# Kernel tuning notes

Hardware: AMD Instinct MI355X
Metric: run time of the kernel (lower is better)

Reference implementation:

```python
import jax, jax.numpy as jnp
import numpy as np

B, T, C, H = 2, 2048, 2048, 16
HD = C // H  # head dim = 128


def setup_inputs() -> dict:
    key = jax.random.key(0)
    k1, k2, k3 = jax.random.split(key, 3)
    x = jax.random.normal(k1, (B, T, C), dtype=jnp.float32)
    # torch Linear stores weight as [out_features, in_features]; y = x @ W.T
    w_attn = jax.random.normal(k2, (3 * C, C), dtype=jnp.float32) * (C ** -0.5)
    w_proj = jax.random.normal(k3, (C, C), dtype=jnp.float32) * (C ** -0.5)
    b_proj = jnp.zeros((C,), dtype=jnp.float32)
    return {"x": x, "w_attn": w_attn, "w_proj": w_proj, "b_proj": b_proj}


def reference(x, w_attn, w_proj, b_proj):
    # c_attn: [B,T,C] -> [B,T,3C], then split into q,k,v
    qkv = jnp.einsum('btc,oc->bto', x, w_attn)
    q, k, v = jnp.split(qkv, 3, axis=-1)
    # [B,T,C] -> [B,H,T,HD]
    q = q.reshape(B, T, H, HD).transpose(0, 2, 1, 3)
    k = k.reshape(B, T, H, HD).transpose(0, 2, 1, 3)
    v = v.reshape(B, T, H, HD).transpose(0, 2, 1, 3)
    scale = 1.0 / jnp.sqrt(jnp.float32(HD))
    att = jnp.einsum('bhqd,bhkd->bhqk', q, k) * scale  # [B,H,T,T]
    causal = jnp.tril(jnp.ones((T, T), dtype=bool))
    att = jnp.where(causal, att, -jnp.inf)
    att = jax.nn.softmax(att, axis=-1)
    # dropout p=0.0 (eval): identity
    y = jnp.einsum('bhqk,bhkd->bhqd', att, v)  # [B,H,T,HD]
    y = y.transpose(0, 2, 1, 3).reshape(B, T, C)
    y = jnp.einsum('btc,oc->bto', y, w_proj) + b_proj
    return y
```

## Files before the change

### kernel.cpp

```cpp
#include <hip/hip_runtime.h>
#include <hip/hip_bf16.h>
#include <stdint.h>
#include <stddef.h>

#define Bn  2
#define Tn  2048
#define Cn  2048
#define Hn  16
#define HDn 128
#define PSTR 140

typedef short short8   __attribute__((ext_vector_type(8)));
typedef short short8_a __attribute__((ext_vector_type(8), may_alias));
typedef unsigned int u32x4_a __attribute__((ext_vector_type(4), may_alias));
typedef unsigned short u16x4_a __attribute__((ext_vector_type(4), may_alias));
typedef unsigned short u16x8_a __attribute__((ext_vector_type(8), may_alias));
typedef float f32x4 __attribute__((ext_vector_type(4)));

typedef __attribute__((address_space(1))) const void av1_t;
typedef __attribute__((address_space(3))) void av3_t;

__device__ inline unsigned short f2b(float f) {
    union { float f; unsigned u; } v; v.f = f;
    unsigned r = v.u + 0x7fffu + ((v.u >> 16) & 1u);
    return (unsigned short)(r >> 16);
}
__device__ inline u16x4_a cvt4_f32_bf16(u32x4_a v) {
    u16x4_a h;
#pragma unroll
    for (int e = 0; e < 4; e++) {
        unsigned u = v[e];
        unsigned r = u + 0x7fffu + ((u >> 16) & 1u);
        h[e] = (unsigned short)(r >> 16);
    }
    return h;
}

__device__ inline void cvt_body(const float* __restrict__ src,
                                unsigned short* __restrict__ dst, int i)
{
    u32x4_a a = *(const u32x4_a*)((const unsigned*)src + i);
    u32x4_a b = *(const u32x4_a*)((const unsigned*)src + i + 4);
    u16x8_a o;
    u16x4_a ha = cvt4_f32_bf16(a), hb = cvt4_f32_bf16(b);
#pragma unroll
    for (int e = 0; e < 4; e++) { o[e] = ha[e]; o[e + 4] = hb[e]; }
    *(u16x8_a*)(dst + i) = o;
}

__global__ __launch_bounds__(256)
void cvt_kernel(const float* __restrict__ src, unsigned short* __restrict__ dst, int n)
{
    const int i = (blockIdx.x * 256 + threadIdx.x) * 8;
    if (i >= n) return;
    cvt_body(src, dst, i);
}

__global__ __launch_bounds__(256)
void cvt2_kernel(const float* __restrict__ s0, unsigned short* __restrict__ d0, int n0,
                 const float* __restrict__ s1, unsigned short* __restrict__ d1, int n1)
{
    int i = (blockIdx.x * 256 + threadIdx.x) * 8;
    if (i < n0) { cvt_body(s0, d0, i); return; }
    i -= n0;
    if (i < n1) cvt_body(s1, d1, i);
}

template<int OUT_F32, int HAS_BIAS>
__global__ __launch_bounds__(256)
void gemm_bb_kernel(const unsigned short* __restrict__ A,
                    const unsigned short* __restrict__ Bm,
                    const float* __restrict__ bias, void* __restrict__ Cv,
                    int M, int N, int K)
{
    __shared__ __align__(16) unsigned short As[128 * 32];
    __shared__ __align__(16) unsigned short Bs[128 * 32];

    const int tid  = threadIdx.x;
    const int lane = tid & 63;
    const int wave = tid >> 6;
    const int quad = lane >> 4;
    const int l15  = lane & 15;
    const int tm = blockIdx.x * 128;
    const int tn = blockIdx.y * 128;
    const int wr = (wave >> 1) * 64;
    const int wc = (wave & 1) * 64;

    const int srow = lane >> 2;
    const int scol = (lane & 3) * 8;

    f32x4 acc[4][4];
#pragma unroll
    for (int i = 0; i < 4; i++)
#pragma unroll
        for (int j = 0; j < 4; j++) acc[i][j] = (f32x4){0.f, 0.f, 0.f, 0.f};

    const int ksteps = K >> 5;
    for (int kt = 0; kt < ksteps; ++kt) {
        const int k0 = kt << 5;
#pragma unroll
        for (int r = 0; r < 2; r++) {
            const int row = (r * 4 + wave) * 16 + srow;
            __builtin_amdgcn_global_load_lds(
                (av1_t*)(A + (size_t)(tm + row) * K + k0 + scol),
                (av3_t*)(&As[row * 32 + scol]), 16, 0, 0);
            __builtin_amdgcn_global_load_lds(
                (av1_t*)(Bm + (size_t)(tn + row) * K + k0 + scol),
                (av3_t*)(&Bs[row * 32 + scol]), 16, 0, 0);
        }
        asm volatile("s_waitcnt vmcnt(0)" ::: "memory");
        __syncthreads();

        short8 af[4], bf[4];
#pragma unroll
        for (int i = 0; i < 4; i++)
            af[i] = (short8)(*(const short8_a*)&As[(wr + i * 16 + l15) * 32 + quad * 8]);
#pragma unroll
        for (int j = 0; j < 4; j++)
            bf[j] = (short8)(*(const short8_a*)&Bs[(wc + j * 16 + l15) * 32 + quad * 8]);
#pragma unroll
        for (int i = 0; i < 4; i++)
#pragma unroll
            for (int j = 0; j < 4; j++)
                acc[i][j] = __builtin_amdgcn_mfma_f32_16x16x32_bf16(af[i], bf[j], acc[i][j], 0, 0, 0);
        __syncthreads();
    }

#pragma unroll
    for (int i = 0; i < 4; i++) {
        const int row = tm + wr + i * 16 + quad * 4;
#pragma unroll
        for (int j = 0; j < 4; j++) {
            const int col = tn + wc + j * 16 + l15;
            const float bv = HAS_BIAS ? bias[col] : 0.0f;
#pragma unroll
            for (int r = 0; r < 4; r++) {
                if (OUT_F32)
                    ((float*)Cv)[(size_t)(row + r) * N + col] = acc[i][j][r] + bv;
                else
                    ((unsigned short*)Cv)[(size_t)(row + r) * N + col] = f2b(acc[i][j][r] + bv);
            }
        }
    }
}

#define LA0 0
#define LB0 16384
#define LA1 32768
#define LB1 49152

template<int NBM, int NBN, int MODE>
__global__ __launch_bounds__(512, 2)
void gemm8_kernel(const unsigned short* __restrict__ A,
                  const unsigned short* __restrict__ Bm,
                  const float* __restrict__ bias,
                  unsigned short* __restrict__ qout,
                  unsigned short* __restrict__ kvout,
                  float* __restrict__ fout)
{
    __shared__ __align__(16) unsigned short lds[65536];

    const int tid  = threadIdx.x;
    const int lane = tid & 63;
    const int wave = tid >> 6;
    const int quad = lane >> 4;
    const int l15  = lane & 15;
    const int wrow = wave >> 2;
    const int wcol = wave & 3;
    const int swz  = (l15 & 7) << 3;

    const int bid  = blockIdx.x;
    const int xcd  = bid & 7;
    const int sl   = bid >> 3;
    const int tile = xcd * (NBM * NBN / 8) + sl;
    const int bm   = tile % NBM;
    const int bn   = tile / NBM;
    const int tm   = bm * 256;
    const int tn   = bn * 256;

    const unsigned short* Ab = A  + (size_t)tm * Cn;
    const unsigned short* Bb = Bm + (size_t)tn * Cn;

    f32x4 acc[8][4];
#pragma unroll
    for (int i = 0; i < 8; i++)
#pragma unroll
        for (int j = 0; j < 4; j++) acc[i][j] = (f32x4){0.f, 0.f, 0.f, 0.f};

    auto stage = [&](const unsigned short* g, int kt, int base, int half) {
#pragma unroll
        for (int rr = 0; rr < 2; ++rr) {
            const int idx = rr * 512 + tid;
            const int row = idx >> 3;
            const int ks  = ((idx & 7) * 8) ^ ((row & 7) << 3);
            __builtin_amdgcn_global_load_lds(
                (av1_t*)(g + (size_t)(half * 128 + row) * Cn + kt * 64 + ks),
                (av3_t*)(lds + base + half * 8192 + idx * 8), 16, 0, 0);
        }
    };
    auto lda = [&](int base, int i, int ks) -> short8 {
        return (short8)(*(const short8_a*)&lds[base + (wrow * 128 + i * 16 + l15) * 64
                                               + ((ks * 32 + quad * 8) ^ swz)]);
    };
    auto ldb = [&](int base, int j, int ks) -> short8 {
        return (short8)(*(const short8_a*)&lds[base + (wcol * 64 + j * 16 + l15) * 64
                                               + ((ks * 32 + quad * 8) ^ swz)]);
    };

    stage(Ab, 0, LA0, 0); stage(Ab, 0, LA0, 1);
    stage(Bb, 0, LB0, 0); stage(Bb, 0, LB0, 1);
    stage(Ab, 1, LA1, 0); stage(Ab, 1, LA1, 1);
    asm volatile("s_waitcnt vmcnt(4)" ::: "memory");
    __builtin_amdgcn_s_barrier();

    const int nt = Cn / 64;
    for (int t = 0; t < nt; t += 2) {
        const bool tail = (t + 2 >= nt);
        short8 af[8][2], bf[2][2];

#pragma unroll
        for (int i = 0; i < 4; i++) { af[i][0] = lda(LA0, i, 0); af[i][1] = lda(LA0, i, 1); }
#pragma unroll
        for (int j = 0; j < 2; j++) { bf[j][0] = ldb(LB0, j, 0); bf[j][1] = ldb(LB0, j, 1); }
        stage(Bb, t + 1, LB1, 0);
        __builtin_amdgcn_s_barrier();
        asm volatile("s_waitcnt lgkmcnt(0)" ::: "memory");
        __builtin_amdgcn_s_setprio(1);
#pragma unroll
        for (int ks = 0; ks < 2; ks++)
#pragma unroll
            for (int i = 0; i < 4; i++)
#pragma unroll
                for (int j = 0; j < 2; j++)
                    acc[i][j] = __builtin_amdgcn_mfma_f32_16x16x32_bf16(af[i][ks], bf[j][ks], acc[i][j], 0, 0, 0);
        __builtin_amdgcn_s_setprio(0);
        __builtin_amdgcn_s_barrier();

#pragma unroll
        for (int i = 4; i < 8; i++) { af[i][0] = lda(LA0, i, 0); af[i][1] = lda(LA0, i, 1); }
        stage(Bb, t + 1, LB1, 1);
        __builtin_amdgcn_s_barrier();
        asm volatile("s_waitcnt lgkmcnt(0)" ::: "memory");
        __builtin_amdgcn_s_setprio(1);
#pragma unroll
        for (int ks = 0; ks < 2; ks++)
#pragma unroll
            for (int i = 4; i < 8; i++)
#pragma unroll
                for (int j = 0; j < 2; j++)
                    acc[i][j] = __builtin_amdgcn_mfma_f32_16x16x32_bf16(af[i][ks], bf[j][ks], acc[i][j], 0, 0, 0);
        __builtin_amdgcn_s_setprio(0);
        __builtin_amdgcn_s_barrier();

#pragma unroll
        for (int j = 0; j < 2; j++) { bf[j][0] = ldb(LB0, 2 + j, 0); bf[j][1] = ldb(LB0, 2 + j, 1); }
        if (!tail) stage(Ab, t + 2, LA0, 0);
        __builtin_amdgcn_s_barrier();
        asm volatile("s_waitcnt lgkmcnt(0)" ::: "memory");
        __builtin_amdgcn_s_setprio(1);
#pragma unroll
        for (int ks = 0; ks < 2; ks++)
#pragma unroll
            for (int i = 0; i < 4; i++)
#pragma unroll
                for (int j = 0; j < 2; j++)
                    acc[i][2 + j] = __builtin_amdgcn_mfma_f32_16x16x32_bf16(af[i][ks], bf[j][ks], acc[i][2 + j], 0, 0, 0);
        __builtin_amdgcn_s_setprio(0);
        __builtin_amdgcn_s_barrier();

        if (!tail) stage(Ab, t + 2, LA0, 1);
        __builtin_amdgcn_s_barrier();
        __builtin_amdgcn_s_setprio(1);
#pragma unroll
        for (int ks = 0; ks < 2; ks++)
#pragma unroll
            for (int i = 4; i < 8; i++)
#pragma unroll
                for (int j = 0; j < 2; j++)
                    acc[i][2 + j] = __builtin_amdgcn_mfma_f32_16x16x32_bf16(af[i][ks], bf[j][ks], acc[i][2 + j], 0, 0, 0);
        __builtin_amdgcn_s_setprio(0);
        if (tail) asm volatile("s_waitcnt vmcnt(0)" ::: "memory");
        else      asm volatile("s_waitcnt vmcnt(4)" ::: "memory");
        __builtin_amdgcn_s_barrier();

#pragma unroll
        for (int i = 0; i < 4; i++) { af[i][0] = lda(LA1, i, 0); af[i][1] = lda(LA1, i, 1); }
#pragma unroll
        for (int j = 0; j < 2; j++) { bf[j][0] = ldb(LB1, j, 0); bf[j][1] = ldb(LB1, j, 1); }
        if (!tail) stage(Bb, t + 2, LB0, 0);
        __builtin_amdgcn_s_barrier();
        asm volatile("s_waitcnt lgkmcnt(0)" ::: "memory");
        __builtin_amdgcn_s_setprio(1);
#pragma unroll
        for (int ks = 0; ks < 2; ks++)
#pragma unroll
            for (int i = 0; i < 4; i++)
#pragma unroll
                for (int j = 0; j < 2; j++)
                    acc[i][j] = __builtin_amdgcn_mfma_f32_16x16x32_bf16(af[i][ks], bf[j][ks], acc[i][j], 0, 0, 0);
        __builtin_amdgcn_s_setprio(0);
        __builtin_amdgcn_s_barrier();

#pragma unroll
        for (int i = 4; i < 8; i++) { af[i][0] = lda(LA1, i, 0); af[i][1] = lda(LA1, i, 1); }
        if (!tail) stage(Bb, t + 2, LB0, 1);
        __builtin_amdgcn_s_barrier();
        asm volatile("s_waitcnt lgkmcnt(0)" ::: "memory");
        __builtin_amdgcn_s_setprio(1);
#pragma unroll
        for (int ks = 0; ks < 2; ks++)
#pragma unroll
            for (int i = 4; i < 8; i++)
#pragma unroll
                for (int j = 0; j < 2; j++)
                    acc[i][j] = __builtin_amdgcn_mfma_f32_16x16x32_bf16(af[i][ks], bf[j][ks], acc[i][j], 0, 0, 0);
        __builtin_amdgcn_s_setprio(0);
        __builtin_amdgcn_s_barrier();

#pragma unroll
        for (int j = 0; j < 2; j++) { bf[j][0] = ldb(LB1, 2 + j, 0); bf[j][1] = ldb(LB1, 2 + j, 1); }
        if (!tail) stage(Ab, t + 3, LA1, 0);
        __builtin_amdgcn_s_barrier();
        asm volatile("s_waitcnt lgkmcnt(0)" ::: "memory");
        __builtin_amdgcn_s_setprio(1);
#pragma unroll
        for (int ks = 0; ks < 2; ks++)
#pragma unroll
            for (int i = 0; i < 4; i++)
#pragma unroll
                for (int j = 0; j < 2; j++)
                    acc[i][2 + j] = __builtin_amdgcn_mfma_f32_16x16x32_bf16(af[i][ks], bf[j][ks], acc[i][2 + j], 0, 0, 0);
        __builtin_amdgcn_s_setprio(0);
        __builtin_amdgcn_s_barrier();

        if (!tail) stage(Ab, t + 3, LA1, 1);
        __builtin_amdgcn_s_barrier();
        __builtin_amdgcn_s_setprio(1);
#pragma unroll
        for (int ks = 0; ks < 2; ks++)
#pragma unroll
            for (int i = 4; i < 8; i++)
#pragma unroll
                for (int j = 0; j < 2; j++)
                    acc[i][2 + j] = __builtin_amdgcn_mfma_f32_16x16x32_bf16(af[i][ks], bf[j][ks], acc[i][2 + j], 0, 0, 0);
        __builtin_amdgcn_s_setprio(0);
        if (tail) asm volatile("s_waitcnt vmcnt(0)" ::: "memory");
        else      asm volatile("s_waitcnt vmcnt(4)" ::: "memory");
        __builtin_amdgcn_s_barrier();
    }

    if (MODE == 0) {
        unsigned short* obase = (tn < Cn) ? qout : kvout;
        const int cofs    = (tn < Cn) ? 0 : Cn;
        const size_t ostr = (tn < Cn) ? Cn : 2 * Cn;
#pragma unroll
        for (int i = 0; i < 8; i++) {
            const int row = tm + wrow * 128 + i * 16 + quad * 4;
#pragma unroll
            for (int j = 0; j < 4; j++) {
                const int col = tn + wcol * 64 + j * 16 + l15 - cofs;
#pragma unroll
                for (int r = 0; r < 4; r++)
                    obase[(size_t)(row + r) * ostr + col] = f2b(acc[i][j][r]);
            }
        }
    } else {
        const int Nn = NBN * 256;
#pragma unroll
        for (int i = 0; i < 8; i++) {
            const int row = tm + wrow * 128 + i * 16 + quad * 4;
#pragma unroll
            for (int j = 0; j < 4; j++) {
                const int col = tn + wcol * 64 + j * 16 + l15;
                const float bv = bias[col];
#pragma unroll
                for (int r = 0; r < 4; r++)
                    fout[(size_t)(row + r) * Nn + col] = acc[i][j][r] + bv;
            }
        }
    }
}

__global__ __launch_bounds__(512, 2)
void attn_kernel(const unsigned short* __restrict__ q,
                 const unsigned short* __restrict__ kv,
                 unsigned short* __restrict__ outp)
{
    __shared__ __align__(16) unsigned short Ks[128 * 136];
    __shared__ __align__(16) unsigned short Vs[128 * 136];
    __shared__ __align__(16) unsigned short Ps[8][16 * PSTR];

    const int bid  = blockIdx.x;
    const int qp   = (bid >> 3) & 7;
    const int bh   = (bid & 7) * 4 + (bid >> 6);
    const int b    = bh >> 4;
    const int h    = bh & 15;
    const int tid  = threadIdx.x;
    const int lane = tid & 63;
    const int wave = tid >> 6;
    const int quad = lane >> 4;
    const int l15  = lane & 15;

    short8 ones;
#pragma unroll
    for (int e = 0; e < 8; e++) ones[e] = (short)0x3F80;

    for (int half = 0; half < 2; ++half) {
        const int qt = half ? (15 - qp) : qp;
        const int qrow0 = qt * 128 + wave * 16;

        short8 qf[4];
#pragma unroll
        for (int kk = 0; kk < 4; kk++) {
            const unsigned short* p = q + (size_t)(b * Tn + qrow0 + l15) * Cn
                                      + h * HDn + kk * 32 + quad * 8;
            qf[kk] = (short8)(*(const short8_a*)p);
        }

        float m_i[4], l_i[4];
        f32x4 o_acc[8];
#pragma unroll
        for (int r = 0; r < 4; r++) { m_i[r] = -1e30f; l_i[r] = 0.f; }
#pragma unroll
        for (int jd = 0; jd < 8; jd++) o_acc[jd] = (f32x4){0.f, 0.f, 0.f, 0.f};

        const int ktiles = qt + 1;

        u32x4_a kr[4], vr[4];
        auto preload = [&](int kt2) {
            const int kk0 = kt2 * 128;
#pragma unroll
            for (int rep = 0; rep < 4; ++rep) {
                const int idx  = tid + rep * 512;
                const int krow = idx >> 4;
                const int dg   = (idx & 15) * 8;
                const size_t rb = (size_t)(b * Tn + kk0 + krow) * (2 * Cn) + h * HDn + dg;
                kr[rep] = *(const u32x4_a*)(kv + rb);
                vr[rep] = *(const u32x4_a*)(kv + rb + Cn);
            }
        };
        preload(0);

        for (int kt2 = 0; kt2 < ktiles; ++kt2) {
            const int kk0 = kt2 * 128;
            __syncthreads();
#pragma unroll
            for (int rep = 0; rep < 4; ++rep) {
                const int idx  = tid + rep * 512;
                const int krow = idx >> 4;
                const int l    = idx & 15;
                const int dg   = l * 8;
                *(u32x4_a*)&Ks[krow * 136 + dg] = kr[rep];
                const int pcol = krow ^ ((l & 7) << 3);
                const unsigned short* ve = (const unsigned short*)&vr[rep];
#pragma unroll
                for (int e = 0; e < 8; e++) Vs[(dg + e) * 136 + pcol] = ve[e];
            }
            __syncthreads();
            if (kt2 + 1 < ktiles) preload(kt2 + 1);

            f32x4 s[8];
#pragma unroll
            for (int j = 0; j < 8; j++) s[j] = (f32x4){0.f, 0.f, 0.f, 0.f};
            __builtin_amdgcn_s_setprio(1);
#pragma unroll
            for (int kk = 0; kk < 4; ++kk) {
                short8 kf[8];
#pragma unroll
                for (int j = 0; j < 8; j++)
                    kf[j] = (short8)(*(const short8_a*)&Ks[(j * 16 + l15) * 136 + kk * 32 + quad * 8]);
#pragma unroll
                for (int j = 0; j < 8; j++)
                    s[j] = __builtin_amdgcn_mfma_f32_16x16x32_bf16(qf[kk], kf[j], s[j], 0, 0, 0);
            }
            __builtin_amdgcn_s_setprio(0);

            const bool needmask = (kk0 + 127 > qrow0);
            float alr[4];
#pragma unroll
            for (int r = 0; r < 4; r++) {
                const int qidx = qrow0 + quad * 4 + r;
                float mx = -1e30f;
#pragma unroll
                for (int j = 0; j < 8; j++) {
                    float v = s[j][r] * 0.08838834764831845f;
                    if (needmask) {
                        const int kidx = kk0 + j * 16 + l15;
                        v = (kidx <= qidx) ? v : -1e30f;
                    }
                    s[j][r] = v;
                    mx = fmaxf(mx, v);
                }
#pragma unroll
                for (int off = 1; off < 16; off <<= 1)
                    mx = fmaxf(mx, __shfl_xor(mx, off));
                const float mn = fmaxf(m_i[r], mx);
                alr[r] = __expf(fminf(m_i[r] - mn, 0.f));
                m_i[r] = mn;
#pragma unroll
                for (int j = 0; j < 8; j++) {
                    const float p = __expf(fminf(s[j][r] - mn, 0.f));
                    s[j][r] = p;
                }
#pragma unroll
                for (int jd = 0; jd < 8; jd++) o_acc[jd][r] *= alr[r];
#pragma unroll
                for (int j = 0; j < 8; j++)
                    Ps[wave][(quad * 4 + r) * PSTR + j * 16 + l15] = f2b(s[j][r]);
            }
            asm volatile("s_waitcnt lgkmcnt(0)" ::: "memory");

            f32x4 lacc = (f32x4){0.f, 0.f, 0.f, 0.f};
            __builtin_amdgcn_s_setprio(1);
#pragma unroll
            for (int kk2 = 0; kk2 < 4; ++kk2) {
                short8 pf = (short8)(*(const short8_a*)&Ps[wave][l15 * PSTR + kk2 * 32 + quad * 8]);
#pragma unroll
                for (int jd = 0; jd < 8; jd++) {
                    const int d = jd * 16 + l15;
                    const int g = (d >> 3) & 7;
                    const int colb = ((4 * kk2 + quad) ^ g) * 8;
                    short8 vf = (short8)(*(const short8_a*)&Vs[d * 136 + colb]);
                    o_acc[jd] = __builtin_amdgcn_mfma_f32_16x16x32_bf16(pf, vf, o_acc[jd], 0, 0, 0);
                }
                lacc = __builtin_amdgcn_mfma_f32_16x16x32_bf16(pf, ones, lacc, 0, 0, 0);
            }
            __builtin_amdgcn_s_setprio(0);
#pragma unroll
            for (int r = 0; r < 4; r++)
                l_i[r] = l_i[r] * alr[r] + lacc[r];
        }

#pragma unroll
        for (int r = 0; r < 4; r++) {
            const float inv = 1.0f / fmaxf(l_i[r], 1e-20f);
            const int trow = qrow0 + quad * 4 + r;
#pragma unroll
            for (int jd = 0; jd < 8; jd++) {
                const int col = h * HDn + jd * 16 + l15;
                outp[(size_t)(b * Tn + trow) * Cn + col] = f2b(o_acc[jd][r] * inv);
            }
        }
    }
}

extern "C" void kernel_launch(void* const* d_in, const int* in_sizes, int n_in,
                              void* d_out, int out_size, void* d_ws, size_t ws_size,
                              hipStream_t stream)
{
    const float* x      = (const float*)d_in[0];
    const float* w_attn = (const float*)d_in[1];
    const float* w_proj = (const float*)d_in[2];
    const float* b_proj = (const float*)d_in[3];
    float* out = (float*)d_out;

    const size_t MiB = 1024 * 1024;
    unsigned short* kvbuf = (unsigned short*)d_out;

    const int nx   = Bn * Tn * Cn;
    const int nwq  = Cn * Cn;
    const int nwkv = 2 * Cn * Cn;

    if (ws_size >= 56 * MiB) {
        unsigned short* xb   = (unsigned short*)d_ws;
        unsigned short* qbuf = (unsigned short*)((char*)d_ws + 16 * MiB);
        unsigned short* wb   = (unsigned short*)((char*)d_ws + 32 * MiB);
        const int nwa = 3 * Cn * Cn;

        cvt2_kernel<<<(nx + nwa) / 8 / 256, 256, 0, stream>>>(x, xb, nx, w_attn, wb, nwa);
        gemm8_kernel<16, 16, 0><<<dim3(256), 512, 0, stream>>>(xb, wb, nullptr,
                                                               qbuf, kvbuf, nullptr);
        gemm_bb_kernel<0, 0><<<dim3(32, 16), 256, 0, stream>>>(
            xb, wb + (size_t)2 * Cn * Cn, nullptr, kvbuf + Cn,
            Bn * Tn, 2 * Cn, Cn);
        attn_kernel<<<dim3(256), 512, 0, stream>>>(qbuf, kvbuf, qbuf);
        cvt_kernel<<<nwq / 8 / 256, 256, 0, stream>>>(w_proj, wb, nwq);
        gemm_bb_kernel<1, 1><<<dim3(32, 16), 256, 0, stream>>>(qbuf, wb, b_proj, out,
                                                               Bn * Tn, Cn, Cn);
    } else {
        unsigned short* xb   = (unsigned short*)d_ws;
        unsigned short* qbuf = (unsigned short*)((char*)d_ws + 16 * MiB);
        unsigned short* wb   = (unsigned short*)((char*)d_ws + 32 * MiB);

        cvt_kernel<<<nx / 8 / 256, 256, 0, stream>>>(x, xb, nx);
        cvt_kernel<<<nwq / 8 / 256, 256, 0, stream>>>(w_attn, wb, nwq);
        gemm_bb_kernel<0, 0><<<dim3(32, 16), 256, 0, stream>>>(xb, wb, nullptr, qbuf,
                                                               Bn * Tn, Cn, Cn);
        cvt_kernel<<<nwkv / 8 / 256, 256, 0, stream>>>(w_attn + (size_t)Cn * Cn, wb, nwkv);
        gemm_bb_kernel<0, 0><<<dim3(32, 32), 256, 0, stream>>>(xb, wb, nullptr, kvbuf,
                                                               Bn * Tn, 2 * Cn, Cn);
        attn_kernel<<<dim3(256), 512, 0, stream>>>(qbuf, kvbuf, qbuf);
        cvt_kernel<<<nwq / 8 / 256, 256, 0, stream>>>(w_proj, wb, nwq);
        gemm_bb_kernel<1, 1><<<dim3(32, 16), 256, 0, stream>>>(qbuf, wb, b_proj, out,
                                                               Bn * Tn, Cn, Cn);
    }
}
```

Before: 387.6 us.

## Split attention q-tile pairs across blocks and alias P with K in shared memory

```diff
diff --git a/kernel.cpp b/kernel.cpp
--- a/kernel.cpp
+++ b/kernel.cpp
@@ -381,20 +381,26 @@
     }
 }
 
-__global__ __launch_bounds__(512, 2)
+__global__ __launch_bounds__(512, 4)
 void attn_kernel(const unsigned short* __restrict__ q,
                  const unsigned short* __restrict__ kv,
                  unsigned short* __restrict__ outp)
 {
-    __shared__ __align__(16) unsigned short Ks[128 * 136];
-    __shared__ __align__(16) unsigned short Vs[128 * 136];
-    __shared__ __align__(16) unsigned short Ps[8][16 * PSTR];
-
-    const int bid  = blockIdx.x;
-    const int qp   = (bid >> 3) & 7;
-    const int bh   = (bid & 7) * 4 + (bid >> 6);
-    const int b    = bh >> 4;
-    const int h    = bh & 15;
+    __shared__ __align__(16) unsigned short smem[35328];
+    unsigned short* Ksm = smem;
+    unsigned short* Psm = smem;
+    unsigned short* Vsm = smem + 17920;
+
+    const int bid   = blockIdx.x;
+    const int low   = bid & 255;
+    const int half  = bid >> 8;
+    const int xcd   = low & 7;
+    const int qslot = (low >> 3) & 7;
+    const int bh    = xcd * 4 + (low >> 6);
+    const int b     = bh >> 4;
+    const int h     = bh & 15;
+    const int qt    = half ? (15 - qslot) : qslot;
+
     const int tid  = threadIdx.x;
     const int lane = tid & 63;
     const int wave = tid >> 6;
@@ -405,141 +411,139 @@
 #pragma unroll
     for (int e = 0; e < 8; e++) ones[e] = (short)0x3F80;
 
-    for (int half = 0; half < 2; ++half) {
-        const int qt = half ? (15 - qp) : qp;
-        const int qrow0 = qt * 128 + wave * 16;
-
-        short8 qf[4];
-#pragma unroll
-        for (int kk = 0; kk < 4; kk++) {
-            const unsigned short* p = q + (size_t)(b * Tn + qrow0 + l15) * Cn
-                                      + h * HDn + kk * 32 + quad * 8;
-            qf[kk] = (short8)(*(const short8_a*)p);
-        }
-
-        float m_i[4], l_i[4];
-        f32x4 o_acc[8];
-#pragma unroll
-        for (int r = 0; r < 4; r++) { m_i[r] = -1e30f; l_i[r] = 0.f; }
-#pragma unroll
-        for (int jd = 0; jd < 8; jd++) o_acc[jd] = (f32x4){0.f, 0.f, 0.f, 0.f};
-
-        const int ktiles = qt + 1;
-
-        u32x4_a kr[4], vr[4];
-        auto preload = [&](int kt2) {
-            const int kk0 = kt2 * 128;
-#pragma unroll
-            for (int rep = 0; rep < 4; ++rep) {
-                const int idx  = tid + rep * 512;
-                const int krow = idx >> 4;
-                const int dg   = (idx & 15) * 8;
-                const size_t rb = (size_t)(b * Tn + kk0 + krow) * (2 * Cn) + h * HDn + dg;
-                kr[rep] = *(const u32x4_a*)(kv + rb);
-                vr[rep] = *(const u32x4_a*)(kv + rb + Cn);
+    const int qrow0 = qt * 128 + wave * 16;
+
+    short8 qf[4];
+#pragma unroll
+    for (int kk = 0; kk < 4; kk++) {
+        const unsigned short* p = q + (size_t)(b * Tn + qrow0 + l15) * Cn
+                                  + h * HDn + kk * 32 + quad * 8;
+        qf[kk] = (short8)(*(const short8_a*)p);
+    }
+
+    float m_i[4], l_i[4];
+    f32x4 o_acc[8];
+#pragma unroll
+    for (int r = 0; r < 4; r++) { m_i[r] = -1e30f; l_i[r] = 0.f; }
+#pragma unroll
+    for (int jd = 0; jd < 8; jd++) o_acc[jd] = (f32x4){0.f, 0.f, 0.f, 0.f};
+
+    const int ktiles = qt + 1;
+
+    u32x4_a kr[4], vr[4];
+    auto preload = [&](int kt2) {
+        const int kk0 = kt2 * 128;
+#pragma unroll
+        for (int rep = 0; rep < 4; ++rep) {
+            const int idx  = tid + rep * 512;
+            const int krow = idx >> 4;
+            const int dg   = (idx & 15) * 8;
+            const size_t rb = (size_t)(b * Tn + kk0 + krow) * (2 * Cn) + h * HDn + dg;
+            kr[rep] = *(const u32x4_a*)(kv + rb);
+            vr[rep] = *(const u32x4_a*)(kv + rb + Cn);
+        }
+    };
+    preload(0);
+
+    for (int kt2 = 0; kt2 < ktiles; ++kt2) {
+        const int kk0 = kt2 * 128;
+        __syncthreads();
+#pragma unroll
+        for (int rep = 0; rep < 4; ++rep) {
+            const int idx  = tid + rep * 512;
+            const int krow = idx >> 4;
+            const int l    = idx & 15;
+            const int dg   = l * 8;
+            *(u32x4_a*)&Ksm[krow * 136 + dg] = kr[rep];
+            const int pcol = krow ^ ((l & 7) << 3);
+            const unsigned short* ve = (const unsigned short*)&vr[rep];
+#pragma unroll
+            for (int e = 0; e < 8; e++) Vsm[(dg + e) * 136 + pcol] = ve[e];
+        }
+        __syncthreads();
+        if (kt2 + 1 < ktiles) preload(kt2 + 1);
+
+        f32x4 s[8];
+#pragma unroll
+        for (int j = 0; j < 8; j++) s[j] = (f32x4){0.f, 0.f, 0.f, 0.f};
+        __builtin_amdgcn_s_setprio(1);
+#pragma unroll
+        for (int kk = 0; kk < 4; ++kk) {
+            short8 kf[8];
+#pragma unroll
+            for (int j = 0; j < 8; j++)
+                kf[j] = (short8)(*(const short8_a*)&Ksm[(j * 16 + l15) * 136 + kk * 32 + quad * 8]);
+#pragma unroll
+            for (int j = 0; j < 8; j++)
+                s[j] = __builtin_amdgcn_mfma_f32_16x16x32_bf16(qf[kk], kf[j], s[j], 0, 0, 0);
+        }
+        __builtin_amdgcn_s_setprio(0);
+        __syncthreads();
+
+        const bool needmask = (kk0 + 127 > qrow0);
+        float alr[4];
+#pragma unroll
+        for (int r = 0; r < 4; r++) {
+            const int qidx = qrow0 + quad * 4 + r;
+            float mx = -1e30f;
+#pragma unroll
+            for (int j = 0; j < 8; j++) {
+                float v = s[j][r] * 0.08838834764831845f;
+                if (needmask) {
+                    const int kidx = kk0 + j * 16 + l15;
+                    v = (kidx <= qidx) ? v : -1e30f;
+                }
+                s[j][r] = v;
+                mx = fmaxf(mx, v);
             }
-        };
-        preload(0);
-
-        for (int kt2 = 0; kt2 < ktiles; ++kt2) {
-            const int kk0 = kt2 * 128;
-            __syncthreads();
-#pragma unroll
-            for (int rep = 0; rep < 4; ++rep) {
-                const int idx  = tid + rep * 512;
-                const int krow = idx >> 4;
-                const int l    = idx & 15;
-                const int dg   = l * 8;
-                *(u32x4_a*)&Ks[krow * 136 + dg] = kr[rep];
-                const int pcol = krow ^ ((l & 7) << 3);
-                const unsigned short* ve = (const unsigned short*)&vr[rep];
-#pragma unroll
-                for (int e = 0; e < 8; e++) Vs[(dg + e) * 136 + pcol] = ve[e];
+#pragma unroll
+            for (int off = 1; off < 16; off <<= 1)
+                mx = fmaxf(mx, __shfl_xor(mx, off));
+            const float mn = fmaxf(m_i[r], mx);
+            alr[r] = __expf(fminf(m_i[r] - mn, 0.f));
+            m_i[r] = mn;
+#pragma unroll
+            for (int j = 0; j < 8; j++) {
+                const float p = __expf(fminf(s[j][r] - mn, 0.f));
+                s[j][r] = p;
             }
-            __syncthreads();
-            if (kt2 + 1 < ktiles) preload(kt2 + 1);
-
-            f32x4 s[8];
-#pragma unroll
-            for (int j = 0; j < 8; j++) s[j] = (f32x4){0.f, 0.f, 0.f, 0.f};
-            __builtin_amdgcn_s_setprio(1);
-#pragma unroll
-            for (int kk = 0; kk < 4; ++kk) {
-                short8 kf[8];
-#pragma unroll
-                for (int j = 0; j < 8; j++)
-                    kf[j] = (short8)(*(const short8_a*)&Ks[(j * 16 + l15) * 136 + kk * 32 + quad * 8]);
-#pragma unroll
-                for (int j = 0; j < 8; j++)
-                    s[j] = __builtin_amdgcn_mfma_f32_16x16x32_bf16(qf[kk], kf[j], s[j], 0, 0, 0);
+#pragma unroll
+            for (int jd = 0; jd < 8; jd++) o_acc[jd][r] *= alr[r];
+#pragma unroll
+            for (int j = 0; j < 8; j++)
+                Psm[wave * 16 * PSTR + (quad * 4 + r) * PSTR + j * 16 + l15] = f2b(s[j][r]);
+        }
+        asm volatile("s_waitcnt lgkmcnt(0)" ::: "memory");
+
+        f32x4 lacc = (f32x4){0.f, 0.f, 0.f, 0.f};
+        __builtin_amdgcn_s_setprio(1);
+#pragma unroll
+        for (int kk2 = 0; kk2 < 4; ++kk2) {
+            short8 pf = (short8)(*(const short8_a*)&Psm[wave * 16 * PSTR + l15 * PSTR + kk2 * 32 + quad * 8]);
+#pragma unroll
+            for (int jd = 0; jd < 8; jd++) {
+                const int d = jd * 16 + l15;
+                const int g = (d >> 3) & 7;
+                const int colb = ((4 * kk2 + quad) ^ g) * 8;
+                short8 vf = (short8)(*(const short8_a*)&Vsm[d * 136 + colb]);
+                o_acc[jd] = __builtin_amdgcn_mfma_f32_16x16x32_bf16(pf, vf, o_acc[jd], 0, 0, 0);
             }
-            __builtin_amdgcn_s_setprio(0);
-
-            const bool needmask = (kk0 + 127 > qrow0);
-            float alr[4];
-#pragma unroll
-            for (int r = 0; r < 4; r++) {
-                const int qidx = qrow0 + quad * 4 + r;
-                float mx = -1e30f;
-#pragma unroll
-                for (int j = 0; j < 8; j++) {
-                    float v = s[j][r] * 0.08838834764831845f;
-                    if (needmask) {
-                        const int kidx = kk0 + j * 16 + l15;
-                        v = (kidx <= qidx) ? v : -1e30f;
-                    }
-                    s[j][r] = v;
-                    mx = fmaxf(mx, v);
-                }
-#pragma unroll
-                for (int off = 1; off < 16; off <<= 1)
-                    mx = fmaxf(mx, __shfl_xor(mx, off));
-                const float mn = fmaxf(m_i[r], mx);
-                alr[r] = __expf(fminf(m_i[r] - mn, 0.f));
-                m_i[r] = mn;
-#pragma unroll
-                for (int j = 0; j < 8; j++) {
-                    const float p = __expf(fminf(s[j][r] - mn, 0.f));
-                    s[j][r] = p;
-                }
-#pragma unroll
-                for (int jd = 0; jd < 8; jd++) o_acc[jd][r] *= alr[r];
-#pragma unroll
-                for (int j = 0; j < 8; j++)
-                    Ps[wave][(quad * 4 + r) * PSTR + j * 16 + l15] = f2b(s[j][r]);
-            }
-            asm volatile("s_waitcnt lgkmcnt(0)" ::: "memory");
-
-            f32x4 lacc = (f32x4){0.f, 0.f, 0.f, 0.f};
-            __builtin_amdgcn_s_setprio(1);
-#pragma unroll
-            for (int kk2 = 0; kk2 < 4; ++kk2) {
-                short8 pf = (short8)(*(const short8_a*)&Ps[wave][l15 * PSTR + kk2 * 32 + quad * 8]);
-#pragma unroll
-                for (int jd = 0; jd < 8; jd++) {
-                    const int d = jd * 16 + l15;
-                    const int g = (d >> 3) & 7;
-                    const int colb = ((4 * kk2 + quad) ^ g) * 8;
-                    short8 vf = (short8)(*(const short8_a*)&Vs[d * 136 + colb]);
-                    o_acc[jd] = __builtin_amdgcn_mfma_f32_16x16x32_bf16(pf, vf, o_acc[jd], 0, 0, 0);
-                }
-                lacc = __builtin_amdgcn_mfma_f32_16x16x32_bf16(pf, ones, lacc, 0, 0, 0);
-            }
-            __builtin_amdgcn_s_setprio(0);
-#pragma unroll
-            for (int r = 0; r < 4; r++)
-                l_i[r] = l_i[r] * alr[r] + lacc[r];
-        }
-
-#pragma unroll
-        for (int r = 0; r < 4; r++) {
-            const float inv = 1.0f / fmaxf(l_i[r], 1e-20f);
-            const int trow = qrow0 + quad * 4 + r;
-#pragma unroll
-            for (int jd = 0; jd < 8; jd++) {
-                const int col = h * HDn + jd * 16 + l15;
-                outp[(size_t)(b * Tn + trow) * Cn + col] = f2b(o_acc[jd][r] * inv);
-            }
+            lacc = __builtin_amdgcn_mfma_f32_16x16x32_bf16(pf, ones, lacc, 0, 0, 0);
+        }
+        __builtin_amdgcn_s_setprio(0);
+#pragma unroll
+        for (int r = 0; r < 4; r++)
+            l_i[r] = l_i[r] * alr[r] + lacc[r];
+    }
+
+#pragma unroll
+    for (int r = 0; r < 4; r++) {
+        const float inv = 1.0f / fmaxf(l_i[r], 1e-20f);
+        const int trow = qrow0 + quad * 4 + r;
+#pragma unroll
+        for (int jd = 0; jd < 8; jd++) {
+            const int col = h * HDn + jd * 16 + l15;
+            outp[(size_t)(b * Tn + trow) * Cn + col] = f2b(o_acc[jd][r] * inv);
         }
     }
 }
@@ -573,7 +577,7 @@
         gemm_bb_kernel<0, 0><<<dim3(32, 16), 256, 0, stream>>>(
             xb, wb + (size_t)2 * Cn * Cn, nullptr, kvbuf + Cn,
             Bn * Tn, 2 * Cn, Cn);
-        attn_kernel<<<dim3(256), 512, 0, stream>>>(qbuf, kvbuf, qbuf);
+        attn_kernel<<<dim3(512), 512, 0, stream>>>(qbuf, kvbuf, qbuf);
         cvt_kernel<<<nwq / 8 / 256, 256, 0, stream>>>(w_proj, wb, nwq);
         gemm_bb_kernel<1, 1><<<dim3(32, 16), 256, 0, stream>>>(qbuf, wb, b_proj, out,
                                                                Bn * Tn, Cn, Cn);
@@ -589,7 +593,7 @@
         cvt_kernel<<<nwkv / 8 / 256, 256, 0, stream>>>(w_attn + (size_t)Cn * Cn, wb, nwkv);
         gemm_bb_kernel<0, 0><<<dim3(32, 32), 256, 0, stream>>>(xb, wb, nullptr, kvbuf,
                                                                Bn * Tn, 2 * Cn, Cn);
-        attn_kernel<<<dim3(256), 512, 0, stream>>>(qbuf, kvbuf, qbuf);
+        attn_kernel<<<dim3(512), 512, 0, stream>>>(qbuf, kvbuf, qbuf);
         cvt_kernel<<<nwq / 8 / 256, 256, 0, stream>>>(w_proj, wb, nwq);
         gemm_bb_kernel<1, 1><<<dim3(32, 16), 256, 0, stream>>>(qbuf, wb, b_proj, out,
                                                                Bn * Tn, Cn, Cn);
```

New measurement: 561.7 us. 1.45x slower.
